# Kernel optimization log

Measured on AMD Instinct MI355X. Metric: run time of the kernel, lower is better.

The kernel has to match this reference:

```python
import jax, jax.numpy as jnp
import numpy as np

N = 10000       # nodes
E = 320000      # edges (avg degree 32)
F_IN = 128      # node_in_fts
F_OUT = 128     # node_out_fts
H = 4           # num_heads_node
E_IN = 64       # edge_in_fts
HOPS = 3        # nr_of_hops
SLOPE = 0.2     # LeakyReLU negative slope (GAT default)


def setup_inputs() -> dict:
    key = jax.random.key(0)
    ks = jax.random.split(key, 10)
    s = 0.05
    return {
        "node_fts": jax.random.normal(ks[0], (N, F_IN), dtype=jnp.float32),
        "edge_fts": jax.random.normal(ks[1], (E, E_IN), dtype=jnp.float32),
        "edges": jax.random.randint(ks[2], (2, E), 0, N),
        # per-hop GATConv params (all hops share dims, stacked on axis 0)
        "Ws": jax.random.normal(ks[3], (HOPS, F_IN, H * F_OUT), dtype=jnp.float32) * s,
        "Wes": jax.random.normal(ks[4], (HOPS, E_IN, H * F_OUT), dtype=jnp.float32) * s,
        "a_src": jax.random.normal(ks[5], (HOPS, H, F_OUT), dtype=jnp.float32) * s,
        "a_dst": jax.random.normal(ks[6], (HOPS, H, F_OUT), dtype=jnp.float32) * s,
        "a_edge": jax.random.normal(ks[7], (HOPS, H, F_OUT), dtype=jnp.float32) * s,
        # gated residual params
        "W_prior": jax.random.normal(ks[8], (F_OUT, F_OUT), dtype=jnp.float32) * s,
        "W_curr": jax.random.normal(ks[9], (F_OUT, F_OUT), dtype=jnp.float32) * s,
    }


def _gat_conv(x, edge_fts, src, dst, W, We, asrc, adst, aedge):
    # dense projections: [N,H,F_OUT] and [E,H,F_OUT]
    h = (x @ W).reshape(-1, H, F_OUT)
    he = (edge_fts @ We).reshape(-1, H, F_OUT)
    h_src = h[src]                                   # [E,H,F_OUT] gather
    # per-edge attention logits [E,H]
    alpha = (h_src * asrc).sum(-1) + (h[dst] * adst).sum(-1) + (he * aedge).sum(-1)
    alpha = jax.nn.leaky_relu(alpha, SLOPE)
    # segment softmax over incoming edges of each destination node
    amax = jnp.full((N, H), -jnp.inf, dtype=alpha.dtype).at[dst].max(alpha)
    w = jnp.exp(alpha - amax[dst])                   # [E,H]
    denom = jax.ops.segment_sum(w, dst, num_segments=N) + 1e-16  # [N,H]
    msg = w[:, :, None] * h_src                      # [E,H,F_OUT]
    out = jax.ops.segment_sum(msg, dst, num_segments=N) / denom[:, :, None]
    return out.mean(axis=1)                          # mean head aggregation -> [N,F_OUT]


def reference(node_fts, edge_fts, edges, Ws, Wes, a_src, a_dst, a_edge, W_prior, W_curr):
    src, dst = edges[0], edges[1]
    x = node_fts
    prior = None
    for i in range(HOPS):
        curr = _gat_conv(x, edge_fts, src, dst, Ws[i], Wes[i], a_src[i], a_dst[i], a_edge[i])
        if prior is None:
            x = curr
        else:
            gate = jax.nn.sigmoid(prior @ W_prior + curr @ W_curr)
            x = gate * curr + (1.0 - gate) * prior
        prior = x
    return x
```

## Files before the change

### kernel.cpp

```cpp
#include <hip/hip_runtime.h>
#include <hip/hip_fp16.h>

#define N_NODES 10000
#define E_EDGES 320000
#define NH 4
#define HOPS 3
#define WMAX 128

typedef _Float16 f16x8 __attribute__((ext_vector_type(8)));
typedef _Float16 f16x4 __attribute__((ext_vector_type(4)));
typedef float    f32x4 __attribute__((ext_vector_type(4)));

__global__ void k_count(const int* __restrict__ dst, int* __restrict__ counts){
  int e = blockIdx.x*256 + threadIdx.x;
  if(e < E_EDGES) atomicAdd(&counts[dst[e]], 1);
}

__global__ __launch_bounds__(1024) void k_scan(const int* __restrict__ counts,
                                               int* __restrict__ row_ptr, int* __restrict__ fillp){
  __shared__ int sm[1024];
  int t = threadIdx.x;
  const int CH = 10;
  int base = t*CH;
  int loc[CH]; int sum = 0;
  #pragma unroll
  for(int i=0;i<CH;i++){
    int v = (base+i < N_NODES) ? counts[base+i] : 0;
    loc[i] = sum; sum += v;
  }
  sm[t] = sum; __syncthreads();
  for(int off=1; off<1024; off<<=1){
    int add = (t>=off) ? sm[t-off] : 0;
    __syncthreads();
    sm[t] += add;
    __syncthreads();
  }
  int excl = (t>0) ? sm[t-1] : 0;
  #pragma unroll
  for(int i=0;i<CH;i++){
    int n = base+i;
    if(n < N_NODES){
      int e = excl + loc[i];
      row_ptr[n] = e;
      fillp[n]   = e;
    }
  }
  if(t==1023) row_ptr[N_NODES] = sm[1023];
}

__global__ void k_fill(const int* __restrict__ src, const int* __restrict__ dst,
                       int* __restrict__ fillp, int* __restrict__ pos_e, int* __restrict__ sorted_src){
  int e = blockIdx.x*256 + threadIdx.x;
  if(e < E_EDGES){
    int d = dst[e];
    int pos = atomicAdd(&fillp[d], 1);
    pos_e[e] = pos;
    sorted_src[pos] = src[e];
  }
}

__global__ __launch_bounds__(256) void k_setup(const float* __restrict__ node_fts, _Float16* __restrict__ xh,
                       const float* __restrict__ Ws, _Float16* __restrict__ WsT,
                       const float* __restrict__ Wes, const float* __restrict__ a_edge,
                       float* __restrict__ b_edge){
  __shared__ float lds[32][65];
  int b = blockIdx.x, t = threadIdx.x;
  if(b < 1250){
    int i = b*256 + t;
    float4 v = *(const float4*)(node_fts + (size_t)i*4);
    f16x4 h = { (_Float16)v.x, (_Float16)v.y, (_Float16)v.z, (_Float16)v.w };
    *(f16x4*)(xh + (size_t)i*4) = h;
  } else if(b < 1346){
    int b2 = b - 1250;
    int hop = b2>>5, rem = b2&31, kt = rem>>3, ct = rem&7;
    int k0 = kt*32, c0 = ct*64;
    const float* wsrc = Ws + (size_t)hop*65536;
    #pragma unroll
    for(int i=0;i<8;i++){
      int u = t + i*256;
      int kk = u>>6, cc = u&63;
      lds[kk][cc] = wsrc[(size_t)(k0+kk)*512 + c0 + cc];
    }
    __syncthreads();
    _Float16* wdst = WsT + (size_t)hop*512*128;
    #pragma unroll
    for(int i=0;i<2;i++){
      int u = t + i*256;
      int c = u>>3, kq = (u&7)*4;
      f16x4 h = { (_Float16)lds[kq][c], (_Float16)lds[kq+1][c],
                  (_Float16)lds[kq+2][c], (_Float16)lds[kq+3][c] };
      *(f16x4*)(wdst + (size_t)(c0+c)*128 + k0 + kq) = h;
    }
  } else {
    int idx = (b-1346)*256 + t;
    if(idx < HOPS*64*NH){
      int hop = idx/(64*NH); int c = (idx/NH)%64; int h = idx%NH;
      const float* we = Wes + (size_t)hop*64*512 + (size_t)c*512 + h*128;
      const float* ae = a_edge + (size_t)hop*NH*128 + h*128;
      float s = 0.f;
      for(int f=0; f<128; f++) s += we[f] * ae[f];
      b_edge[idx] = s;
    }
  }
}

__global__ __launch_bounds__(256) void k_alpha_e(const float* __restrict__ edge_fts,
                        const int* __restrict__ pos_e, const float* __restrict__ b_edge,
                        float* __restrict__ ae_sorted){
  __shared__ float bl[HOPS*64*NH];
  for(int i=threadIdx.x; i<HOPS*64*NH; i+=256) bl[i] = b_edge[i];
  __syncthreads();
  int t = threadIdx.x;
  int el = t>>1, half = t&1;
  int e = blockIdx.x*128 + el;
  float acc[HOPS*NH];
  #pragma unroll
  for(int i=0;i<HOPS*NH;i++) acc[i]=0.f;
  const float* ef = edge_fts + (size_t)e*64 + half*32;
  const float* blh = bl + half*128;
  #pragma unroll 2
  for(int c=0; c<32; c+=4){
    float4 xv = *(const float4*)(ef + c);
    float x[4] = {xv.x, xv.y, xv.z, xv.w};
    #pragma unroll
    for(int j=0;j<4;j++){
      float xc = x[j]; int cc = c+j;
      #pragma unroll
      for(int hh=0; hh<HOPS*NH; hh++){
        int hop = hh>>2, h = hh&3;
        acc[hh] += xc * blh[hop*256 + cc*4 + h];
      }
    }
  }
  #pragma unroll
  for(int hh=0; hh<HOPS*NH; hh++) acc[hh] += __shfl_xor(acc[hh], 1);
  int pos = pos_e[e];
  if(half==0){
    *(float4*)(ae_sorted + ((size_t)0*E_EDGES + pos)*4) = make_float4(acc[0],acc[1],acc[2],acc[3]);
    *(float4*)(ae_sorted + ((size_t)2*E_EDGES + pos)*4) = make_float4(acc[8],acc[9],acc[10],acc[11]);
  } else {
    *(float4*)(ae_sorted + ((size_t)1*E_EDGES + pos)*4) = make_float4(acc[4],acc[5],acc[6],acc[7]);
  }
}

__global__ __launch_bounds__(256) void k_projm(const _Float16* __restrict__ xh,
                       const _Float16* __restrict__ Wt, __half* __restrict__ h_all){
  __shared__ __align__(16) __half tile[64][72];
  int w = threadIdx.x>>6, l = threadIdx.x&63;
  int rowb = blockIdx.x*64;
  int row0 = rowb + w*16;
  int col0 = blockIdx.y*64;
  int ar = l&15, ac = (l>>4)*8;
  f32x4 acc0 = {0.f,0.f,0.f,0.f}, acc1 = acc0, acc2 = acc0, acc3 = acc0;
  #pragma unroll
  for(int kk=0; kk<4; kk++){
    f16x8 a  = *(const f16x8*)(xh + (size_t)(row0+ar)*128 + kk*32 + ac);
    f16x8 b0 = *(const f16x8*)(Wt + (size_t)(col0 +  0 + ar)*128 + kk*32 + ac);
    f16x8 b1 = *(const f16x8*)(Wt + (size_t)(col0 + 16 + ar)*128 + kk*32 + ac);
    f16x8 b2 = *(const f16x8*)(Wt + (size_t)(col0 + 32 + ar)*128 + kk*32 + ac);
    f16x8 b3 = *(const f16x8*)(Wt + (size_t)(col0 + 48 + ar)*128 + kk*32 + ac);
    acc0 = __builtin_amdgcn_mfma_f32_16x16x32_f16(a, b0, acc0, 0, 0, 0);
    acc1 = __builtin_amdgcn_mfma_f32_16x16x32_f16(a, b1, acc1, 0, 0, 0);
    acc2 = __builtin_amdgcn_mfma_f32_16x16x32_f16(a, b2, acc2, 0, 0, 0);
    acc3 = __builtin_amdgcn_mfma_f32_16x16x32_f16(a, b3, acc3, 0, 0, 0);
  }
  int crow = (l>>4)*4, ccol = l&15;
  #pragma unroll
  for(int r=0; r<4; r++){
    int tr = w*16 + crow + r;
    tile[tr][ccol     ] = __float2half(acc0[r]);
    tile[tr][ccol + 16] = __float2half(acc1[r]);
    tile[tr][ccol + 32] = __float2half(acc2[r]);
    tile[tr][ccol + 48] = __float2half(acc3[r]);
  }
  __syncthreads();
  #pragma unroll
  for(int i=0;i<2;i++){
    int u = threadIdx.x + i*256;
    int row = u>>3, cq = (u&7)*8;
    int grow = rowb + row;
    if(grow < N_NODES)
      *(float4*)(h_all + (size_t)grow*512 + col0 + cq) = *(const float4*)&tile[row][cq];
  }
}

__global__ __launch_bounds__(256) void k_s(const __half* __restrict__ h_all, const float* __restrict__ asrc,
                    const float* __restrict__ adst, float* __restrict__ s_src, float* __restrict__ s_dst){
  int nw = blockIdx.x*4 + (threadIdx.x>>6);
  int l = threadIdx.x&63;
  if(nw >= N_NODES) return;
  int h = l>>4, f8 = (l&15)*8;
  const __half* hp = h_all + (size_t)nw*512 + (h<<7) + f8;
  float4 raw = *(const float4*)hp;
  const __half2* hh = (const __half2*)&raw;
  float2 c0 = __half22float2(hh[0]);
  float2 c1 = __half22float2(hh[1]);
  float2 c2 = __half22float2(hh[2]);
  float2 c3 = __half22float2(hh[3]);
  float4 a0 = *(const float4*)(asrc + (h<<7) + f8);
  float4 a1 = *(const float4*)(asrc + (h<<7) + f8 + 4);
  float4 d0 = *(const float4*)(adst + (h<<7) + f8);
  float4 d1 = *(const float4*)(adst + (h<<7) + f8 + 4);
  float ps = c0.x*a0.x + c0.y*a0.y + c1.x*a0.z + c1.y*a0.w
           + c2.x*a1.x + c2.y*a1.y + c3.x*a1.z + c3.y*a1.w;
  float pd = c0.x*d0.x + c0.y*d0.y + c1.x*d0.z + c1.y*d0.w
           + c2.x*d1.x + c2.y*d1.y + c3.x*d1.z + c3.y*d1.w;
  #pragma unroll
  for(int off=1; off<16; off<<=1){ ps += __shfl_xor(ps,off); pd += __shfl_xor(pd,off); }
  if((l&15)==0){ s_src[nw*4+h] = ps; s_dst[nw*4+h] = pd; }
}

__global__ __launch_bounds__(256) void k_softagg(
    const float* __restrict__ ae, const float* __restrict__ s_src,
    const float* __restrict__ s_dst, const int* __restrict__ sorted_src,
    const int* __restrict__ row_ptr, const __half* __restrict__ h_all,
    float* __restrict__ ew_fb, float* __restrict__ xout, _Float16* __restrict__ xh)
{
  __shared__ float ws4[4][WMAX*4];
  __shared__ int   ssm4[4][WMAX];
  int wv = threadIdx.x>>6, l = threadIdx.x&63;
  int n = blockIdx.x*4 + wv;
  if(n >= N_NODES) return;
  int start = row_ptr[n], end = row_ptr[n+1];
  int deg = end - start;
  bool fits = (deg <= WMAX);
  float* ws = ws4[wv];
  int*   ssm = ssm4[wv];

  float4 sd = *(const float4*)(s_dst + (size_t)n*4);
  float m0=-1e30f, m1=-1e30f, m2=-1e30f, m3=-1e30f;
  float aR[2][4];

  if(fits){
    #pragma unroll
    for(int k=0;k<2;k++){
      int idx = l + k*64;
      if(idx < deg){
        int pos = start + idx;
        int s = sorted_src[pos];
        float4 ss = *(const float4*)(s_src + (size_t)s*4);
        float4 av = *(const float4*)(ae + (size_t)pos*4);
        float a0 = ss.x+sd.x+av.x; a0=(a0>0.f)?a0:0.2f*a0;
        float a1 = ss.y+sd.y+av.y; a1=(a1>0.f)?a1:0.2f*a1;
        float a2 = ss.z+sd.z+av.z; a2=(a2>0.f)?a2:0.2f*a2;
        float a3 = ss.w+sd.w+av.w; a3=(a3>0.f)?a3:0.2f*a3;
        aR[k][0]=a0; aR[k][1]=a1; aR[k][2]=a2; aR[k][3]=a3;
        ssm[idx] = s;
        m0=fmaxf(m0,a0); m1=fmaxf(m1,a1); m2=fmaxf(m2,a2); m3=fmaxf(m3,a3);
      }
    }
  } else {
    for(int pos=start+l; pos<end; pos+=64){
      int s = sorted_src[pos];
      float4 ss = *(const float4*)(s_src + (size_t)s*4);
      float4 av = *(const float4*)(ae + (size_t)pos*4);
      float a0 = ss.x+sd.x+av.x; a0=(a0>0.f)?a0:0.2f*a0;
      float a1 = ss.y+sd.y+av.y; a1=(a1>0.f)?a1:0.2f*a1;
      float a2 = ss.z+sd.z+av.z; a2=(a2>0.f)?a2:0.2f*a2;
      float a3 = ss.w+sd.w+av.w; a3=(a3>0.f)?a3:0.2f*a3;
      *(float4*)(ew_fb + (size_t)pos*4) = make_float4(a0,a1,a2,a3);
      m0=fmaxf(m0,a0); m1=fmaxf(m1,a1); m2=fmaxf(m2,a2); m3=fmaxf(m3,a3);
    }
  }
  #pragma unroll
  for(int off=32; off; off>>=1){
    m0=fmaxf(m0,__shfl_xor(m0,off)); m1=fmaxf(m1,__shfl_xor(m1,off));
    m2=fmaxf(m2,__shfl_xor(m2,off)); m3=fmaxf(m3,__shfl_xor(m3,off));
  }

  float s0=0.f,s1=0.f,s2=0.f,s3=0.f;
  if(fits){
    #pragma unroll
    for(int k=0;k<2;k++){
      int idx = l + k*64;
      if(idx < deg){
        float w0=__expf(aR[k][0]-m0), w1=__expf(aR[k][1]-m1);
        float w2=__expf(aR[k][2]-m2), w3=__expf(aR[k][3]-m3);
        int sl = idx*4;
        ws[sl]=w0; ws[sl+1]=w1; ws[sl+2]=w2; ws[sl+3]=w3;
        s0+=w0; s1+=w1; s2+=w2; s3+=w3;
      }
    }
  } else {
    for(int pos=start+l; pos<end; pos+=64){
      float4 a = *(const float4*)(ew_fb + (size_t)pos*4);
      float w0=__expf(a.x-m0), w1=__expf(a.y-m1), w2=__expf(a.z-m2), w3=__expf(a.w-m3);
      *(float4*)(ew_fb + (size_t)pos*4) = make_float4(w0,w1,w2,w3);
      s0+=w0; s1+=w1; s2+=w2; s3+=w3;
    }
  }
  #pragma unroll
  for(int off=32; off; off>>=1){
    s0+=__shfl_xor(s0,off); s1+=__shfl_xor(s1,off);
    s2+=__shfl_xor(s2,off); s3+=__shfl_xor(s3,off);
  }

  int h = l>>4, f8 = (l&15)*8;
  float dh = (h==0)?s0:((h==1)?s1:((h==2)?s2:s3));
  float inv = 1.f/(dh + 1e-16f);
  float acc[8] = {0.f,0.f,0.f,0.f,0.f,0.f,0.f,0.f};
  for(int sl=0; sl<deg; sl++){
    int s; float w;
    if(fits){ s = ssm[sl]; w = ws[sl*4 + h]; }
    else    { s = sorted_src[start+sl]; w = ew_fb[(size_t)(start+sl)*4 + h]; }
    const __half* hp = h_all + (size_t)s*512 + (h<<7) + f8;
    float4 raw = *(const float4*)hp;
    const __half2* hh = (const __half2*)&raw;
    float2 c0 = __half22float2(hh[0]);
    float2 c1 = __half22float2(hh[1]);
    float2 c2 = __half22float2(hh[2]);
    float2 c3 = __half22float2(hh[3]);
    acc[0]+=w*c0.x; acc[1]+=w*c0.y; acc[2]+=w*c1.x; acc[3]+=w*c1.y;
    acc[4]+=w*c2.x; acc[5]+=w*c2.y; acc[6]+=w*c3.x; acc[7]+=w*c3.y;
  }
  #pragma unroll
  for(int i=0;i<8;i++){
    acc[i] *= inv;
    acc[i] += __shfl_xor(acc[i], 16);
    acc[i] += __shfl_xor(acc[i], 32);
    acc[i] *= 0.25f;
  }
  if(l < 16){
    int f0 = l*8;
    *(float4*)(xout + (size_t)n*128 + f0)     = make_float4(acc[0],acc[1],acc[2],acc[3]);
    *(float4*)(xout + (size_t)n*128 + f0 + 4) = make_float4(acc[4],acc[5],acc[6],acc[7]);
    if(xh){
      f16x8 hv = { (_Float16)acc[0],(_Float16)acc[1],(_Float16)acc[2],(_Float16)acc[3],
                   (_Float16)acc[4],(_Float16)acc[5],(_Float16)acc[6],(_Float16)acc[7] };
      *(f16x8*)(xh + (size_t)n*128 + f0) = hv;
    }
  }
}

__global__ __launch_bounds__(256) void k_gate2(const float* __restrict__ prior, const float* __restrict__ curr,
                       const float* __restrict__ Wp, const float* __restrict__ Wc,
                       float* __restrict__ xnew, _Float16* __restrict__ xh){
  __shared__ float pr[32][132];
  __shared__ float cu[32][132];
  int t = threadIdx.x;
  int n0 = blockIdx.x*32;
  int c0 = blockIdx.y*64;
  #pragma unroll
  for(int i=0;i<4;i++){
    int u = t + i*256;
    int row = u>>5, c4 = (u&31)<<2;
    float4 v = make_float4(0.f,0.f,0.f,0.f), w = v;
    if(n0+row < N_NODES){
      v = *(const float4*)(prior + (size_t)(n0+row)*128 + c4);
      w = *(const float4*)(curr  + (size_t)(n0+row)*128 + c4);
    }
    *(float4*)&pr[row][c4] = v;
    *(float4*)&cu[row][c4] = w;
  }
  __syncthreads();
  int tc = t&15, tr = t>>4;
  int r0 = tr*2, cc = c0 + tc*4;
  float accp[2][4] = {{0.f,0.f,0.f,0.f},{0.f,0.f,0.f,0.f}};
  float accc[2][4] = {{0.f,0.f,0.f,0.f},{0.f,0.f,0.f,0.f}};
  #pragma unroll 4
  for(int k=0;k<128;k++){
    float4 wp = *(const float4*)(Wp + (size_t)k*128 + cc);
    float4 wc = *(const float4*)(Wc + (size_t)k*128 + cc);
    #pragma unroll
    for(int i=0;i<2;i++){
      float ap = pr[r0+i][k], ac = cu[r0+i][k];
      accp[i][0]+=ap*wp.x; accp[i][1]+=ap*wp.y; accp[i][2]+=ap*wp.z; accp[i][3]+=ap*wp.w;
      accc[i][0]+=ac*wc.x; accc[i][1]+=ac*wc.y; accc[i][2]+=ac*wc.z; accc[i][3]+=ac*wc.w;
    }
  }
  #pragma unroll
  for(int i=0;i<2;i++){
    int row = n0 + r0 + i;
    if(row < N_NODES){
      float oj[4];
      #pragma unroll
      for(int j=0;j<4;j++){
        float z = accp[i][j]+accc[i][j];
        float g = 1.f/(1.f+__expf(-z));
        oj[j] = g*cu[r0+i][cc + j] + (1.f-g)*pr[r0+i][cc + j];
      }
      *(float4*)(xnew + (size_t)row*128 + cc) = make_float4(oj[0],oj[1],oj[2],oj[3]);
      if(xh){
        f16x4 hv = { (_Float16)oj[0], (_Float16)oj[1], (_Float16)oj[2], (_Float16)oj[3] };
        *(f16x4*)(xh + (size_t)row*128 + cc) = hv;
      }
    }
  }
}

extern "C" void kernel_launch(void* const* d_in, const int* in_sizes, int n_in,
                              void* d_out, int out_size, void* d_ws, size_t ws_size,
                              hipStream_t stream){
  (void)in_sizes; (void)n_in; (void)out_size; (void)ws_size;
  const float* node_fts = (const float*)d_in[0];
  const float* edge_fts = (const float*)d_in[1];
  const int*   edges    = (const int*)d_in[2];
  const float* Ws       = (const float*)d_in[3];
  const float* Wes      = (const float*)d_in[4];
  const float* a_src    = (const float*)d_in[5];
  const float* a_dst    = (const float*)d_in[6];
  const float* a_edge   = (const float*)d_in[7];
  const float* W_prior  = (const float*)d_in[8];
  const float* W_curr   = (const float*)d_in[9];

  char* ws = (char*)d_ws;
  size_t off = 0;
  auto alloc = [&](size_t bytes)->void*{
    void* p = ws + off;
    off += (bytes + 255) & ~(size_t)255;
    return p;
  };
  int*       counts     = (int*)      alloc((size_t)N_NODES*4);
  int*       row_ptr    = (int*)      alloc((size_t)(N_NODES+1)*4);
  int*       fillp      = (int*)      alloc((size_t)N_NODES*4);
  int*       pos_e      = (int*)      alloc((size_t)E_EDGES*4);
  int*       sorted_src = (int*)      alloc((size_t)E_EDGES*4);
  float*     b_edge     = (float*)    alloc((size_t)HOPS*64*NH*4);
  float*     ae_sorted  = (float*)    alloc((size_t)HOPS*E_EDGES*NH*4);
  __half*    h_all      = (__half*)   alloc((size_t)N_NODES*512*2);
  float*     s_src      = (float*)    alloc((size_t)N_NODES*NH*4);
  float*     s_dst      = (float*)    alloc((size_t)N_NODES*NH*4);
  float*     ew_fb      = (float*)    alloc((size_t)E_EDGES*NH*4);
  float*     xbuf       = (float*)    alloc((size_t)N_NODES*128*4);
  float*     curbuf     = (float*)    alloc((size_t)N_NODES*128*4);
  _Float16*  xh         = (_Float16*) alloc((size_t)10112*128*2);
  _Float16*  WsT        = (_Float16*) alloc((size_t)HOPS*512*128*2);

  const int* src = edges;
  const int* dst = edges + E_EDGES;

  (void)hipMemsetAsync(counts, 0, (size_t)N_NODES*4, stream);
  k_count<<<(E_EDGES+255)/256, 256, 0, stream>>>(dst, counts);
  k_scan<<<1, 1024, 0, stream>>>(counts, row_ptr, fillp);
  k_fill<<<(E_EDGES+255)/256, 256, 0, stream>>>(src, dst, fillp, pos_e, sorted_src);
  k_setup<<<1349, 256, 0, stream>>>(node_fts, xh, Ws, WsT, Wes, a_edge, b_edge);
  k_alpha_e<<<2500, 256, 0, stream>>>(edge_fts, pos_e, b_edge, ae_sorted);

  for(int hop=0; hop<HOPS; hop++){
    k_projm<<<dim3(157, 8), 256, 0, stream>>>(xh, WsT + (size_t)hop*512*128, h_all);
    k_s<<<2500, 256, 0, stream>>>(h_all, a_src + (size_t)hop*512, a_dst + (size_t)hop*512, s_src, s_dst);
    float* xout = (hop==0) ? xbuf : curbuf;
    k_softagg<<<2500, 256, 0, stream>>>(ae_sorted + (size_t)hop*E_EDGES*4, s_src, s_dst,
                                        sorted_src, row_ptr, h_all, ew_fb, xout,
                                        (hop==0) ? xh : (_Float16*)nullptr);
    if(hop > 0){
      float* xnew = (hop == HOPS-1) ? (float*)d_out : xbuf;
      k_gate2<<<dim3(313, 2), 256, 0, stream>>>(xbuf, curbuf, W_prior, W_curr, xnew,
                                                (hop < HOPS-1) ? xh : (_Float16*)nullptr);
    }
  }
}
```

Measured before the change: 347.5 us.

## Compute edge attention logits with MFMA in natural edge order, gather via CSR edge ids

Replaces the scalar per-edge logit projection with a 16x16x32 fp16 MFMA kernel that writes all hops' edge logits in original edge order as 16 floats per edge. The fill kernel now records the original edge id per CSR slot instead of each edge's sorted position. The softmax-aggregate kernel reads logits indirectly through that id. This removes scattered writes and the scalar FMA work in the logit kernel, at the cost of an extra index load and a non-coalesced gather per edge in every hop, plus fp16 rounding of edge features and weights.

Measured after the change: 345.8 us. About the same (-0.5%).

```diff
diff --git a/kernel.cpp b/kernel.cpp
--- a/kernel.cpp
+++ b/kernel.cpp
@@ -49,12 +49,12 @@
 }
 
 __global__ void k_fill(const int* __restrict__ src, const int* __restrict__ dst,
-                       int* __restrict__ fillp, int* __restrict__ pos_e, int* __restrict__ sorted_src){
+                       int* __restrict__ fillp, int* __restrict__ csr_eid, int* __restrict__ sorted_src){
   int e = blockIdx.x*256 + threadIdx.x;
   if(e < E_EDGES){
     int d = dst[e];
     int pos = atomicAdd(&fillp[d], 1);
-    pos_e[e] = pos;
+    csr_eid[pos] = e;
     sorted_src[pos] = src[e];
   }
 }
@@ -104,43 +104,50 @@
   }
 }
 
-__global__ __launch_bounds__(256) void k_alpha_e(const float* __restrict__ edge_fts,
-                        const int* __restrict__ pos_e, const float* __restrict__ b_edge,
-                        float* __restrict__ ae_sorted){
-  __shared__ float bl[HOPS*64*NH];
-  for(int i=threadIdx.x; i<HOPS*64*NH; i+=256) bl[i] = b_edge[i];
+__global__ __launch_bounds__(256) void k_alpha_mfma(const float* __restrict__ edge_fts,
+                        const float* __restrict__ b_edge, float* __restrict__ ae_nat){
+  __shared__ float tile[64][20];
+  int w = threadIdx.x>>6, l = threadIdx.x&63;
+  int col = l&15, kgrp = l>>4;
+  f16x8 bf0, bf1;
+  #pragma unroll
+  for(int j=0;j<8;j++){
+    int k0 = 0*32 + kgrp*8 + j;
+    int k1 = 1*32 + kgrp*8 + j;
+    float v0 = 0.f, v1 = 0.f;
+    if(col < 12){
+      int hop = col>>2, h = col&3;
+      v0 = b_edge[hop*256 + k0*4 + h];
+      v1 = b_edge[hop*256 + k1*4 + h];
+    }
+    bf0[j] = (_Float16)v0;
+    bf1[j] = (_Float16)v1;
+  }
+  int e0 = blockIdx.x*64 + w*16;
+  int erow = e0 + (l&15);
+  const float* ef = edge_fts + (size_t)erow*64 + kgrp*8;
+  f32x4 acc = {0.f,0.f,0.f,0.f};
+  {
+    float4 x0 = *(const float4*)(ef);
+    float4 x1 = *(const float4*)(ef + 4);
+    f16x8 a = { (_Float16)x0.x,(_Float16)x0.y,(_Float16)x0.z,(_Float16)x0.w,
+                (_Float16)x1.x,(_Float16)x1.y,(_Float16)x1.z,(_Float16)x1.w };
+    acc = __builtin_amdgcn_mfma_f32_16x16x32_f16(a, bf0, acc, 0, 0, 0);
+  }
+  {
+    float4 x0 = *(const float4*)(ef + 32);
+    float4 x1 = *(const float4*)(ef + 36);
+    f16x8 a = { (_Float16)x0.x,(_Float16)x0.y,(_Float16)x0.z,(_Float16)x0.w,
+                (_Float16)x1.x,(_Float16)x1.y,(_Float16)x1.z,(_Float16)x1.w };
+    acc = __builtin_amdgcn_mfma_f32_16x16x32_f16(a, bf1, acc, 0, 0, 0);
+  }
+  int crow = (l>>4)*4;
+  #pragma unroll
+  for(int r=0;r<4;r++) tile[w*16 + crow + r][col] = acc[r];
   __syncthreads();
-  int t = threadIdx.x;
-  int el = t>>1, half = t&1;
-  int e = blockIdx.x*128 + el;
-  float acc[HOPS*NH];
-  #pragma unroll
-  for(int i=0;i<HOPS*NH;i++) acc[i]=0.f;
-  const float* ef = edge_fts + (size_t)e*64 + half*32;
-  const float* blh = bl + half*128;
-  #pragma unroll 2
-  for(int c=0; c<32; c+=4){
-    float4 xv = *(const float4*)(ef + c);
-    float x[4] = {xv.x, xv.y, xv.z, xv.w};
-    #pragma unroll
-    for(int j=0;j<4;j++){
-      float xc = x[j]; int cc = c+j;
-      #pragma unroll
-      for(int hh=0; hh<HOPS*NH; hh++){
-        int hop = hh>>2, h = hh&3;
-        acc[hh] += xc * blh[hop*256 + cc*4 + h];
-      }
-    }
-  }
-  #pragma unroll
-  for(int hh=0; hh<HOPS*NH; hh++) acc[hh] += __shfl_xor(acc[hh], 1);
-  int pos = pos_e[e];
-  if(half==0){
-    *(float4*)(ae_sorted + ((size_t)0*E_EDGES + pos)*4) = make_float4(acc[0],acc[1],acc[2],acc[3]);
-    *(float4*)(ae_sorted + ((size_t)2*E_EDGES + pos)*4) = make_float4(acc[8],acc[9],acc[10],acc[11]);
-  } else {
-    *(float4*)(ae_sorted + ((size_t)1*E_EDGES + pos)*4) = make_float4(acc[4],acc[5],acc[6],acc[7]);
-  }
+  int u = threadIdx.x;
+  int edge = u>>2, q = u&3;
+  *(float4*)(ae_nat + ((size_t)(blockIdx.x*64 + edge))*16 + q*4) = *(const float4*)&tile[edge][q*4];
 }
 
 __global__ __launch_bounds__(256) void k_projm(const _Float16* __restrict__ xh,
@@ -211,9 +218,10 @@
 }
 
 __global__ __launch_bounds__(256) void k_softagg(
-    const float* __restrict__ ae, const float* __restrict__ s_src,
+    const float* __restrict__ ae_nat, int hop, const float* __restrict__ s_src,
     const float* __restrict__ s_dst, const int* __restrict__ sorted_src,
-    const int* __restrict__ row_ptr, const __half* __restrict__ h_all,
+    const int* __restrict__ csr_eid, const int* __restrict__ row_ptr,
+    const __half* __restrict__ h_all,
     float* __restrict__ ew_fb, float* __restrict__ xout, _Float16* __restrict__ xh)
 {
   __shared__ float ws4[4][WMAX*4];
@@ -238,8 +246,9 @@
       if(idx < deg){
         int pos = start + idx;
         int s = sorted_src[pos];
+        int e = csr_eid[pos];
         float4 ss = *(const float4*)(s_src + (size_t)s*4);
-        float4 av = *(const float4*)(ae + (size_t)pos*4);
+        float4 av = *(const float4*)(ae_nat + (size_t)e*16 + hop*4);
         float a0 = ss.x+sd.x+av.x; a0=(a0>0.f)?a0:0.2f*a0;
         float a1 = ss.y+sd.y+av.y; a1=(a1>0.f)?a1:0.2f*a1;
         float a2 = ss.z+sd.z+av.z; a2=(a2>0.f)?a2:0.2f*a2;
@@ -252,8 +261,9 @@
   } else {
     for(int pos=start+l; pos<end; pos+=64){
       int s = sorted_src[pos];
+      int e = csr_eid[pos];
       float4 ss = *(const float4*)(s_src + (size_t)s*4);
-      float4 av = *(const float4*)(ae + (size_t)pos*4);
+      float4 av = *(const float4*)(ae_nat + (size_t)e*16 + hop*4);
       float a0 = ss.x+sd.x+av.x; a0=(a0>0.f)?a0:0.2f*a0;
       float a1 = ss.y+sd.y+av.y; a1=(a1>0.f)?a1:0.2f*a1;
       float a2 = ss.z+sd.z+av.z; a2=(a2>0.f)?a2:0.2f*a2;
@@ -413,10 +423,10 @@
   int*       counts     = (int*)      alloc((size_t)N_NODES*4);
   int*       row_ptr    = (int*)      alloc((size_t)(N_NODES+1)*4);
   int*       fillp      = (int*)      alloc((size_t)N_NODES*4);
-  int*       pos_e      = (int*)      alloc((size_t)E_EDGES*4);
+  int*       csr_eid    = (int*)      alloc((size_t)E_EDGES*4);
   int*       sorted_src = (int*)      alloc((size_t)E_EDGES*4);
   float*     b_edge     = (float*)    alloc((size_t)HOPS*64*NH*4);
-  float*     ae_sorted  = (float*)    alloc((size_t)HOPS*E_EDGES*NH*4);
+  float*     ae_nat     = (float*)    alloc((size_t)E_EDGES*16*4);
   __half*    h_all      = (__half*)   alloc((size_t)N_NODES*512*2);
   float*     s_src      = (float*)    alloc((size_t)N_NODES*NH*4);
   float*     s_dst      = (float*)    alloc((size_t)N_NODES*NH*4);
@@ -432,16 +442,16 @@
   (void)hipMemsetAsync(counts, 0, (size_t)N_NODES*4, stream);
   k_count<<<(E_EDGES+255)/256, 256, 0, stream>>>(dst, counts);
   k_scan<<<1, 1024, 0, stream>>>(counts, row_ptr, fillp);
-  k_fill<<<(E_EDGES+255)/256, 256, 0, stream>>>(src, dst, fillp, pos_e, sorted_src);
+  k_fill<<<(E_EDGES+255)/256, 256, 0, stream>>>(src, dst, fillp, csr_eid, sorted_src);
   k_setup<<<1349, 256, 0, stream>>>(node_fts, xh, Ws, WsT, Wes, a_edge, b_edge);
-  k_alpha_e<<<2500, 256, 0, stream>>>(edge_fts, pos_e, b_edge, ae_sorted);
+  k_alpha_mfma<<<5000, 256, 0, stream>>>(edge_fts, b_edge, ae_nat);
 
   for(int hop=0; hop<HOPS; hop++){
     k_projm<<<dim3(157, 8), 256, 0, stream>>>(xh, WsT + (size_t)hop*512*128, h_all);
     k_s<<<2500, 256, 0, stream>>>(h_all, a_src + (size_t)hop*512, a_dst + (size_t)hop*512, s_src, s_dst);
     float* xout = (hop==0) ? xbuf : curbuf;
-    k_softagg<<<2500, 256, 0, stream>>>(ae_sorted + (size_t)hop*E_EDGES*4, s_src, s_dst,
-                                        sorted_src, row_ptr, h_all, ew_fb, xout,
+    k_softagg<<<2500, 256, 0, stream>>>(ae_nat, hop, s_src, s_dst,
+                                        sorted_src, csr_eid, row_ptr, h_all, ew_fb, xout,
                                         (hop==0) ? xh : (_Float16*)nullptr);
     if(hop > 0){
       float* xnew = (hop == HOPS-1) ? (float*)d_out : xbuf;
```
